# Optimization experiments

Hardware: AMD Instinct MI355X
Metric: run time of the kernel (lower is better)

## Reference

```python
import jax, jax.numpy as jnp
import numpy as np

N, E, MUL = 10000, 160000, 16
DIM = 9            # sum of 2l+1 for l=0..2
UV = 5             # 2*lmax+1
CONV = 9           # uv1 + uv2 - 1
ONE = CONV // 2 + 1
LOG2 = np.float32(np.log(2.0))


def _ssp(x):
    # ShiftedSoftPlus
    return jax.nn.softplus(x) - LOG2


def _build_a_w():
    # weight_align_matrix scaled by path_w ~ sqrt(2l+1): row l covers its (2l+1) block
    a = np.zeros((3, DIM), dtype=np.float32)
    off = 0
    for l in range(3):
        d = 2 * l + 1
        a[l, off:off + d] = np.sqrt(np.float32(d))
        off += d
    return jnp.asarray(a)


def setup_inputs() -> dict:
    key = jax.random.key(0)
    ks = jax.random.split(key, 14)
    inp = {
        "x": jax.random.normal(ks[0], (N, MUL, DIM), jnp.float32),
        "filter_sph": jax.random.normal(ks[1], (E, DIM), jnp.float32),
        "weight_in": jax.random.uniform(ks[2], (E, 8), jnp.float32),
        "edge_idx": jax.random.randint(ks[3], (2, E), 0, N),
        "Ux_re": jax.random.normal(ks[4], (DIM, UV, UV), jnp.float32),
        "Ux_im": jax.random.normal(ks[5], (DIM, UV, UV), jnp.float32),
        "Uf_re": jax.random.normal(ks[6], (DIM, UV, UV), jnp.float32),
        "Uf_im": jax.random.normal(ks[7], (DIM, UV, UV), jnp.float32),
        "Vout_re": jax.random.normal(ks[8], (CONV, ONE, DIM), jnp.float32),
        "Vout_im": jax.random.normal(ks[9], (CONV, ONE, DIM), jnp.float32),
        "W1": jax.random.normal(ks[10], (8, 64), jnp.float32),
        "W2": jax.random.normal(ks[11], (64, 64), jnp.float32),
        "W3": jax.random.normal(ks[12], (64, MUL * 3), jnp.float32),
        "a_w": _build_a_w(),
        "denominator": jnp.ones((1,), jnp.float32),
    }
    return inp


def _to_grid(coeff, U):
    # coeff [..., DIM] real; U [DIM, UV, UV] complex -> real grid [..., CONV, CONV]
    f = jnp.einsum('...d,duv->...uv', coeff.astype(U.dtype), U)
    pad = (CONV - UV) // 2
    cfg = [(0, 0)] * (f.ndim - 2) + [(pad, pad), (pad, pad)]
    fp = jnp.pad(f, cfg)
    fo = jnp.fft.ifftshift(fp, axes=(-2, -1))[..., :ONE]
    return jnp.fft.irfft2(fo, s=(CONV, CONV), axes=(-2, -1), norm='backward')


def reference(x, filter_sph, weight_in, edge_idx, Ux_re, Ux_im, Uf_re, Uf_im,
              Vout_re, Vout_im, W1, W2, W3, a_w, denominator):
    Ux = jax.lax.complex(Ux_re, Ux_im)
    Uf = jax.lax.complex(Uf_re, Uf_im)
    Vo = jax.lax.complex(Vout_re, Vout_im)
    edge_src = edge_idx[1]
    edge_dst = edge_idx[0]

    # node and filter signals on the CONVxCONV Fourier grid
    xf = _to_grid(x, Ux)                             # [N, MUL, 9, 9]
    yf = _to_grid(filter_sph[:, None, :], Uf)        # [E, 1, 9, 9]

    conv = xf[edge_src] * yf                         # [E, MUL, 9, 9]
    out_f = jnp.fft.rfft2(conv, axes=(-2, -1))       # [E, MUL, 9, 5] complex
    msg = jnp.einsum('emuv,uvd->emd', out_f, Vo).real  # ToSphericalBasis (hermitian input)

    # weight MLP (e3nn FullyConnectedNet: x @ W / sqrt(fan_in), ssp between)
    h = _ssp(weight_in @ W1 * (1.0 / np.sqrt(8.0, dtype=np.float32)))
    h = _ssp(h @ W2 * (1.0 / np.sqrt(64.0, dtype=np.float32)))
    w = (h @ W3 * (1.0 / np.sqrt(64.0, dtype=np.float32))).reshape(-1, MUL, 3)

    factor = jnp.einsum('emp,pd->emd', w, a_w)       # weight @ a_w
    message = msg * factor                           # [E, MUL, 9]

    out = jax.ops.segment_sum(message, edge_dst, num_segments=N)  # scatter-reduce sum
    return out / denominator[0]
```

## Files before the change

kernel.cpp:

```cpp
#include <hip/hip_runtime.h>
#include <math.h>

#define PI9 (2.0f * 3.14159265358979323846f / 9.0f)

typedef float f32x4 __attribute__((ext_vector_type(4)));
typedef unsigned short us8 __attribute__((ext_vector_type(8)));
typedef __bf16 bf16x8 __attribute__((ext_vector_type(8)));
typedef unsigned int u32x4 __attribute__((ext_vector_type(4)));

__device__ __forceinline__ float ssp_f(float x) {
  const float ax = fabsf(x);
  const float t = __expf(-ax);
  return fmaxf(x, 0.f) + __logf(1.f + t) - 0.69314718f;
}

__device__ __forceinline__ unsigned short f2bf(float f) {
  unsigned int u = __float_as_uint(f);
  unsigned int r = (u + 0x7FFFu + ((u >> 16) & 1u)) >> 16;
  return (unsigned short)r;
}

__device__ __forceinline__ float bfLO(unsigned int u) {
  return __uint_as_float(u << 16);
}
__device__ __forceinline__ float bfHI(unsigned int u) {
  return __uint_as_float(u & 0xffff0000u);
}

__global__ __launch_bounds__(256) void wconv_kernel(
    const float* __restrict__ W1, const float* __restrict__ W2,
    const float* __restrict__ W3, const float* __restrict__ a_w,
    const float* __restrict__ den, unsigned short* __restrict__ W1T,
    unsigned short* __restrict__ W2T, unsigned short* __restrict__ W3T,
    int* __restrict__ cnt, int N) {
  const int i = blockIdx.x * 256 + threadIdx.x;
  const float invden = 1.f / den[0];
  const float sc0 = a_w[0] * invden, sc1 = a_w[10] * invden, sc2 = a_w[22] * invden;
  const float rs8 = 0.35355339059327373f;
  if (i < N) cnt[i] = 0;
  if (i < 512) {
    const int col = i & 63, kk = i >> 6;
    W1T[col * 8 + kk] = f2bf(W1[kk * 64 + col] * rs8);
  } else if (i < 4608) {
    const int ii = i - 512;
    const int k = ii >> 6, j = ii & 63;
    W2T[j * 64 + ((((k >> 3) ^ (j & 7)) << 3)) + (k & 7)] = f2bf(W2[ii] * 0.125f);
  } else if (i < 7680) {
    const int ii = i - 4608;
    const int k = ii / 48, j = ii % 48;
    const int jm = j % 3;
    const float s = (jm == 0) ? sc0 : ((jm == 1) ? sc1 : sc2);
    W3T[j * 64 + ((((k >> 3) ^ (j & 7)) << 3)) + (k & 7)] = f2bf(W3[ii] * 0.125f * s);
  }
}

__device__ void precompute_body(
    int d, unsigned char* smem,
    const float* __restrict__ Ux_re, const float* __restrict__ Ux_im,
    const float* __restrict__ Uf_re, const float* __restrict__ Uf_im,
    const float* __restrict__ Vo_re, const float* __restrict__ Vo_im,
    float* __restrict__ CT) {
  float* G = (float*)smem;
  float* TL = (float*)(smem + 5840);
  float* cs9 = (float*)(smem + 8768);
  float* sn9 = (float*)(smem + 8816);
  const int t0 = threadIdx.x;

  if (t0 < 9) {
    float s, c;
    __sincosf(PI9 * (float)t0, &s, &c);
    cs9[t0] = c; sn9[t0] = s;
  }
  __syncthreads();

  for (int t = t0; t < 1458; t += 256) {
    const int which = t / 729, idx = t % 729;
    const int p = idx / 81, ab = idx % 81, a = ab / 9, b = ab % 9;
    const float* Ure = which ? Uf_re : Ux_re;
    const float* Uim = which ? Uf_im : Ux_im;
    float g = 0.f;
#pragma unroll
    for (int v = 0; v < 3; ++v) {
      const int uc = v + 2;
      float hre = 0.f, him = 0.f;
#pragma unroll
      for (int ui = 0; ui < 5; ++ui) {
        const int u = (ui + 7) % 9;
        const float re = Ure[p * 25 + ui * 5 + uc];
        const float im = Uim[p * 25 + ui * 5 + uc];
        const int k = (u * a) % 9;
        const float c = cs9[k], s = sn9[k];
        hre += re * c - im * s;
        him += re * s + im * c;
      }
      hre *= (1.f / 9.f); him *= (1.f / 9.f);
      if (v == 0) {
        g += hre;
      } else {
        const int k = (v * b) % 9;
        g += 2.f * (hre * cs9[k] - him * sn9[k]);
      }
    }
    G[which * 729 + p * 81 + ab] = g * (1.f / 9.f);
  }
  __syncthreads();

  for (int t = t0; t < 729; t += 256) {
    const int ab = t / 9, dd = t % 9, a = ab / 9, b = ab % 9;
    float acc = 0.f;
    for (int u = 0; u < 9; ++u)
      for (int v = 0; v < 5; ++v) {
        const int k = (u * a + v * b) % 9;
        acc += Vo_re[u * 45 + v * 9 + dd] * cs9[k]
             + Vo_im[u * 45 + v * 9 + dd] * sn9[k];
      }
    TL[ab * 9 + dd] = acc;
  }
  __syncthreads();

  if (t0 < 108) {
    const int p = t0 / 12, q = t0 % 12;
    float acc = 0.f;
    if (q < 9) {
      for (int ab = 0; ab < 81; ++ab)
        acc += G[p * 81 + ab] * G[729 + q * 81 + ab] * TL[ab * 9 + d];
    }
    CT[(d * 9 + p) * 12 + q] = acc;
  }
}

__device__ void mlp_body(
    int mblk, unsigned char* smem, const float* __restrict__ win,
    const unsigned short* __restrict__ W1T,
    const unsigned short* __restrict__ W2T,
    const unsigned short* __restrict__ W3T,
    unsigned short* __restrict__ w48b) {
  unsigned short* H1 = (unsigned short*)smem + ((threadIdx.x >> 6) * 1024);
  unsigned short* H2 = (unsigned short*)(smem + 8192) + ((threadIdx.x >> 6) * 1024);
  const int t = threadIdx.x;
  const int w = t >> 6, l = t & 63;
  const int n16 = l & 15, g = l >> 4;
  const bool isg0 = (g == 0);

#pragma unroll 1
  for (int rep = 0; rep < 2; ++rep) {
    const int e = mblk * 128 + rep * 64 + w * 16 + n16;

    bf16x8 Aw;
#pragma unroll
    for (int j = 0; j < 8; ++j) Aw[j] = (__bf16)0.f;
    if (isg0) {
      const float4 A = *(const float4*)(win + (size_t)e * 8);
      const float4 B = *(const float4*)(win + (size_t)e * 8 + 4);
      Aw[0] = (__bf16)A.x; Aw[1] = (__bf16)A.y;
      Aw[2] = (__bf16)A.z; Aw[3] = (__bf16)A.w;
      Aw[4] = (__bf16)B.x; Aw[5] = (__bf16)B.y;
      Aw[6] = (__bf16)B.z; Aw[7] = (__bf16)B.w;
    }
#pragma unroll
    for (int nt = 0; nt < 4; ++nt) {
      const int col = nt * 16 + n16;
      us8 bz;
#pragma unroll
      for (int j = 0; j < 8; ++j) bz[j] = 0;
      const us8 bw = isg0 ? *(const us8*)&W1T[col * 8] : bz;
      f32x4 acc = {0.f, 0.f, 0.f, 0.f};
      acc = __builtin_amdgcn_mfma_f32_16x16x32_bf16(
          Aw, __builtin_bit_cast(bf16x8, bw), acc, 0, 0, 0);
#pragma unroll
      for (int r = 0; r < 4; ++r) {
        const int e2 = g * 4 + r;
        const int k2 = nt * 16 + n16;
        H1[e2 * 64 + ((((k2 >> 3) ^ (e2 & 7)) << 3)) + (k2 & 7)] =
            f2bf(ssp_f(acc[r]));
      }
    }
    __builtin_amdgcn_wave_barrier();

    {
      const us8 a0 = *(const us8*)&H1[n16 * 64 + ((g ^ (n16 & 7)) << 3)];
      const us8 a1 = *(const us8*)&H1[n16 * 64 + (((g + 4) ^ (n16 & 7)) << 3)];
      float hh[16];
#pragma unroll
      for (int nt = 0; nt < 4; ++nt) {
        const int j = nt * 16 + n16;
        const us8 b0 = *(const us8*)&W2T[j * 64 + ((g ^ (j & 7)) << 3)];
        const us8 b1 = *(const us8*)&W2T[j * 64 + (((g + 4) ^ (j & 7)) << 3)];
        f32x4 acc = {0.f, 0.f, 0.f, 0.f};
        acc = __builtin_amdgcn_mfma_f32_16x16x32_bf16(
            __builtin_bit_cast(bf16x8, a0), __builtin_bit_cast(bf16x8, b0), acc, 0, 0, 0);
        acc = __builtin_amdgcn_mfma_f32_16x16x32_bf16(
            __builtin_bit_cast(bf16x8, a1), __builtin_bit_cast(bf16x8, b1), acc, 0, 0, 0);
#pragma unroll
        for (int r = 0; r < 4; ++r) hh[nt * 4 + r] = ssp_f(acc[r]);
      }
#pragma unroll
      for (int nt = 0; nt < 4; ++nt)
#pragma unroll
        for (int r = 0; r < 4; ++r) {
          const int e2 = g * 4 + r;
          const int k2 = nt * 16 + n16;
          H2[e2 * 64 + ((((k2 >> 3) ^ (e2 & 7)) << 3)) + (k2 & 7)] =
              f2bf(hh[nt * 4 + r]);
        }
    }
    __builtin_amdgcn_wave_barrier();

    {
      const us8 c0 = *(const us8*)&H2[n16 * 64 + ((g ^ (n16 & 7)) << 3)];
      const us8 c1 = *(const us8*)&H2[n16 * 64 + (((g + 4) ^ (n16 & 7)) << 3)];
      const int ebase = mblk * 128 + rep * 64 + w * 16 + g * 4;
#pragma unroll
      for (int nt = 0; nt < 3; ++nt) {
        const int o = nt * 16 + n16;
        const int om = o / 3, ol = o - om * 3;
        const us8 b0 = *(const us8*)&W3T[o * 64 + ((g ^ (o & 7)) << 3)];
        const us8 b1 = *(const us8*)&W3T[o * 64 + (((g + 4) ^ (o & 7)) << 3)];
        f32x4 acc = {0.f, 0.f, 0.f, 0.f};
        acc = __builtin_amdgcn_mfma_f32_16x16x32_bf16(
            __builtin_bit_cast(bf16x8, c0), __builtin_bit_cast(bf16x8, b0), acc, 0, 0, 0);
        acc = __builtin_amdgcn_mfma_f32_16x16x32_bf16(
            __builtin_bit_cast(bf16x8, c1), __builtin_bit_cast(bf16x8, b1), acc, 0, 0, 0);
#pragma unroll
        for (int r = 0; r < 4; ++r)
          w48b[(size_t)(ebase + r) * 64 + ol * 16 + om] = f2bf(acc[r]);
      }
    }
    __builtin_amdgcn_wave_barrier();
  }
}

__global__ __launch_bounds__(256) void prep_kernel(
    const float* __restrict__ win, const unsigned short* __restrict__ W1T,
    const unsigned short* __restrict__ W2T,
    const unsigned short* __restrict__ W3T,
    unsigned short* __restrict__ w48b,
    const int* __restrict__ dst, const int* __restrict__ src, int E,
    int* __restrict__ cnt, int2* __restrict__ slots2,
    const float* __restrict__ xsrc, int NR, unsigned short* __restrict__ xbf,
    const float* __restrict__ Ux_re, const float* __restrict__ Ux_im,
    const float* __restrict__ Uf_re, const float* __restrict__ Uf_im,
    const float* __restrict__ Vo_re, const float* __restrict__ Vo_im,
    float* __restrict__ CT, int nMlp, int nScat) {
  __shared__ __align__(16) unsigned char smem[16384];
  const int bid = blockIdx.x;
  if (bid < 9) {
    precompute_body(bid, smem, Ux_re, Ux_im, Uf_re, Uf_im, Vo_re, Vo_im, CT);
  } else if (bid < 9 + nMlp) {
    mlp_body(bid - 9, smem, win, W1T, W2T, W3T, w48b);
  } else if (bid < 9 + nMlp + nScat) {
    const int e = (bid - 9 - nMlp) * 256 + threadIdx.x;
    if (e < E) {
      const int d = dst[e];
      const int pos = atomicAdd(&cnt[d], 1);
      if (pos < 96) slots2[(size_t)d * 96 + pos] = make_int2(e, src[e]);
    }
  } else {
    const int r = (bid - 9 - nMlp - nScat) * 256 + threadIdx.x;
    if (r < NR) {
      const float* xp = xsrc + (size_t)r * 9;
      unsigned int u0 = (unsigned)f2bf(xp[0]) | ((unsigned)f2bf(xp[1]) << 16);
      unsigned int u1 = (unsigned)f2bf(xp[2]) | ((unsigned)f2bf(xp[3]) << 16);
      unsigned int u2 = (unsigned)f2bf(xp[4]) | ((unsigned)f2bf(xp[5]) << 16);
      unsigned int u3 = (unsigned)f2bf(xp[6]) | ((unsigned)f2bf(xp[7]) << 16);
      unsigned int u4 = (unsigned)f2bf(xp[8]);
      unsigned short* op = xbf + (size_t)r * 12;
      *(uint2*)op = make_uint2(u0, u1);
      *(uint2*)(op + 4) = make_uint2(u2, u3);
      *(uint2*)(op + 8) = make_uint2(u4, 0u);
    }
  }
}

__global__ __launch_bounds__(256) void node_kernel(
    const unsigned short* __restrict__ xbf, const float* __restrict__ filt,
    const int* __restrict__ cnt, const int2* __restrict__ slots2,
    const unsigned short* __restrict__ w48b, const float* __restrict__ CT,
    float* __restrict__ out, int N) {
  __shared__ __align__(16) unsigned short meL[4][2304];
  const int t = threadIdx.x, w = t >> 6, l = t & 63;
  const int n16 = l & 15, g = l >> 4;
  const int Ld = (n16 == 0) ? 0 : ((n16 < 4) ? 1 : 2);
  const bool dok = n16 < 9;
  const int drow = dok ? n16 : 0;
  const bool isg0 = (g == 0), isg1 = (g == 1);
  const int n = blockIdx.x * 4 + w;
  if (n >= N) return;

  int dT0, pT0, dT1, pT1, dT2, pT2, dT3, pT3, dT4, pT4, dT5, pT5;
  bool ok0, ok1, ok2, ok3, ok4, ok5;
  bf16x8 Bme0, Bme1, Bme2, Bme3, Bme4, Bme5;
#define MKB(tt, Bv, dv, pv, okv)                                             \
  {                                                                          \
    const int col = tt * 16 + n16;                                           \
    okv = (col < 81);                                                        \
    dv = okv ? col / 9 : 0;                                                  \
    pv = okv ? col % 9 : 0;                                                  \
    bf16x8 bv;                                                               \
    _Pragma("unroll")                                                        \
    for (int j = 0; j < 8; ++j) bv[j] = (__bf16)0.f;                         \
    if (okv) {                                                               \
      const float* cp = CT + col * 12;                                       \
      if (g == 0) {                                                          \
        const float4 ca = *(const float4*)cp;                                \
        const float4 cb = *(const float4*)(cp + 4);                          \
        bv[0] = (__bf16)ca.x; bv[1] = (__bf16)ca.y;                          \
        bv[2] = (__bf16)ca.z; bv[3] = (__bf16)ca.w;                          \
        bv[4] = (__bf16)cb.x; bv[5] = (__bf16)cb.y;                          \
        bv[6] = (__bf16)cb.z; bv[7] = (__bf16)cb.w;                          \
      } else if (g == 1) {                                                   \
        bv[0] = (__bf16)cp[8];                                               \
      }                                                                      \
    }                                                                        \
    Bv = bv;                                                                 \
  }
  MKB(0, Bme0, dT0, pT0, ok0); MKB(1, Bme1, dT1, pT1, ok1);
  MKB(2, Bme2, dT2, pT2, ok2); MKB(3, Bme3, dT3, pT3, ok3);
  MKB(4, Bme4, dT4, pT4, ok4); MKB(5, Bme5, dT5, pT5, ok5);
#undef MKB

  int deg = cnt[n];
  if (deg > 96) deg = 96;
  const int2* sl2 = slots2 + (size_t)n * 96;
  unsigned short* mlw = &meL[w][0];

  f32x4 accm = {0.f, 0.f, 0.f, 0.f};

  const int nb = (deg + 15) >> 4;
  for (int b = 0; b < nb; ++b) {
    const int base = b * 16;
    const int degb = (deg - base < 16) ? (deg - base) : 16;

    int esx = 0, esy = 0;
    if (n16 < degb) {
      const int2 v = sl2[base + n16];
      esx = v.x; esy = v.y;
    }
    bf16x8 Af;
#pragma unroll
    for (int j = 0; j < 8; ++j) Af[j] = (__bf16)0.f;
    if (n16 < degb) {
      const float* fp = filt + (size_t)esx * 9;
      if (g == 0) {
        const float4 fa = *(const float4*)fp;
        const float4 fb = *(const float4*)(fp + 4);
        Af[0] = (__bf16)fa.x; Af[1] = (__bf16)fa.y;
        Af[2] = (__bf16)fa.z; Af[3] = (__bf16)fa.w;
        Af[4] = (__bf16)fb.x; Af[5] = (__bf16)fb.y;
        Af[6] = (__bf16)fb.z; Af[7] = (__bf16)fb.w;
      } else if (g == 1) {
        Af[0] = (__bf16)fp[8];
      }
    }

#define MEMFMA(Bv, dv, pv, okv)                                              \
    {                                                                        \
      f32x4 a6 = {0.f, 0.f, 0.f, 0.f};                                       \
      a6 = __builtin_amdgcn_mfma_f32_16x16x32_bf16(Af, Bv, a6, 0, 0, 0);     \
      if (okv) {                                                             \
        _Pragma("unroll")                                                    \
        for (int r = 0; r < 4; ++r)                                          \
          mlw[(g * 4 + r) * 144 + dv * 16 + pv] = f2bf(a6[r]);               \
      }                                                                      \
    }
    MEMFMA(Bme0, dT0, pT0, ok0); MEMFMA(Bme1, dT1, pT1, ok1);
    MEMFMA(Bme2, dT2, pT2, ok2); MEMFMA(Bme3, dT3, pT3, ok3);
    MEMFMA(Bme4, dT4, pT4, ok4); MEMFMA(Bme5, dT5, pT5, ok5);
#undef MEMFMA
    __builtin_amdgcn_wave_barrier();

#define MSGLOAD(Q, QC, WV, il_)                                              \
    {                                                                        \
      const int e_ = __builtin_amdgcn_readlane(esx, (il_));                  \
      const int s_ = __builtin_amdgcn_readlane(esy, (il_));                  \
      const unsigned short* xrp_ = xbf + (size_t)s_ * 192 + n16 * 12;        \
      Q = *(const u32x4*)xrp_;                                               \
      QC = *(const unsigned int*)(xrp_ + 8);                                 \
      WV = *(const uint2*)(w48b + (size_t)e_ * 64 + Ld * 16 + g * 4);        \
    }

    u32x4 qA, qB;
    unsigned int qcA, qcB;
    uint2 wvA, wvB;
    MSGLOAD(qA, qcA, wvA, 0);
    if (degb > 1) MSGLOAD(qB, qcB, wvB, 1);

#pragma unroll 1
    for (int il = 0; il < degb; ++il) {
      const u32x4 q = qA;
      const unsigned int qc = qcA;
      const uint2 wv = wvA;
      qA = qB; qcA = qcB; wvA = wvB;
      if (il + 2 < degb) MSGLOAD(qB, qcB, wvB, il + 2);

      const unsigned short* mr = mlw + il * 144 + drow * 16;
      const u32x4 mdv = *(const u32x4*)mr;
      const unsigned int md4 = (*(const unsigned int*)(mr + 8)) & 0xffffu;

      u32x4 av;
      av[0] = isg0 ? q[0] : (isg1 ? qc : 0u);
      av[1] = isg0 ? q[1] : 0u;
      av[2] = isg0 ? q[2] : 0u;
      av[3] = isg0 ? q[3] : 0u;
      u32x4 bv;
      bv[0] = isg0 ? mdv[0] : (isg1 ? md4 : 0u);
      bv[1] = isg0 ? mdv[1] : 0u;
      bv[2] = isg0 ? mdv[2] : 0u;
      bv[3] = isg0 ? mdv[3] : 0u;

      f32x4 c1 = {0.f, 0.f, 0.f, 0.f};
      c1 = __builtin_amdgcn_mfma_f32_16x16x32_bf16(
          __builtin_bit_cast(bf16x8, av), __builtin_bit_cast(bf16x8, bv),
          c1, 0, 0, 0);
      accm[0] = fmaf(c1[0], bfLO(wv.x), accm[0]);
      accm[1] = fmaf(c1[1], bfHI(wv.x), accm[1]);
      accm[2] = fmaf(c1[2], bfLO(wv.y), accm[2]);
      accm[3] = fmaf(c1[3], bfHI(wv.y), accm[3]);
    }
#undef MSGLOAD
    __builtin_amdgcn_wave_barrier();
  }

  if (dok) {
    float* op = out + (size_t)n * 144 + (g * 4) * 9 + n16;
    op[0]  = accm[0];
    op[9]  = accm[1];
    op[18] = accm[2];
    op[27] = accm[3];
  }
}

extern "C" void kernel_launch(void* const* d_in, const int* in_sizes, int n_in,
                              void* d_out, int out_size, void* d_ws, size_t ws_size,
                              hipStream_t stream) {
  const float* x      = (const float*)d_in[0];
  const float* filt   = (const float*)d_in[1];
  const float* win    = (const float*)d_in[2];
  const int*   eidx   = (const int*)d_in[3];
  const float* Ux_re  = (const float*)d_in[4];
  const float* Ux_im  = (const float*)d_in[5];
  const float* Uf_re  = (const float*)d_in[6];
  const float* Uf_im  = (const float*)d_in[7];
  const float* Vo_re  = (const float*)d_in[8];
  const float* Vo_im  = (const float*)d_in[9];
  const float* W1     = (const float*)d_in[10];
  const float* W2     = (const float*)d_in[11];
  const float* W3     = (const float*)d_in[12];
  const float* a_w    = (const float*)d_in[13];
  const float* den    = (const float*)d_in[14];
  float* out = (float*)d_out;

  const int N = in_sizes[0] / 144;
  const int E = in_sizes[3] / 2;
  const int NR = N * 16;
  const int* dst = eidx;
  const int* src = eidx + E;

  char* wsb = (char*)d_ws;
  const size_t off_cnt  = 8192;
  const size_t off_slot = off_cnt + 40960;
  const size_t off_w48  = off_slot + (size_t)N * 96 * 8;
  const size_t off_xbf  = off_w48 + (size_t)E * 64 * 2;
  const size_t off_w1t  = off_xbf + (size_t)NR * 12 * 2;
  const size_t off_w2t  = off_w1t + 512 * 2;
  const size_t off_w3t  = off_w2t + 4096 * 2;

  float*          CT    = (float*)wsb;
  int*            cnt   = (int*)(wsb + off_cnt);
  int2*           slot2 = (int2*)(wsb + off_slot);
  unsigned short* w48b  = (unsigned short*)(wsb + off_w48);
  unsigned short* xbf   = (unsigned short*)(wsb + off_xbf);
  unsigned short* W1T   = (unsigned short*)(wsb + off_w1t);
  unsigned short* W2T   = (unsigned short*)(wsb + off_w2t);
  unsigned short* W3T   = (unsigned short*)(wsb + off_w3t);

  const int nMlp  = E / 128;
  const int nScat = (E + 255) / 256;
  const int nXc   = (NR + 255) / 256;

  wconv_kernel<<<(N + 255) / 256, 256, 0, stream>>>(
      W1, W2, W3, a_w, den, W1T, W2T, W3T, cnt, N);
  prep_kernel<<<9 + nMlp + nScat + nXc, 256, 0, stream>>>(
      win, W1T, W2T, W3T, w48b,
      dst, src, E, cnt, slot2,
      x, NR, xbf,
      Ux_re, Ux_im, Uf_re, Uf_im, Vo_re, Vo_im, CT, nMlp, nScat);
  node_kernel<<<(N + 3) / 4, 256, 0, stream>>>(
      xbf, filt, cnt, slot2, w48b, CT, out, N);
}
```

Before: 73.87 us.

## Split MLP blocks finer and software-pipeline node message loop with dual accumulators

The MLP part of prep_kernel now handles 64 edges per block instead of looping twice over 128, which doubles the number of MLP blocks for more parallelism. In node_kernel, the edge slot indices for the next 16-edge batch are prefetched before the barrier. The per-edge message loop is unrolled by two, with the LDS filter loads folded into the prefetch and two independent accumulators to break the FMA dependency chain. This adds register pressure and more blocks in exchange for better latency hiding.

```diff
diff --git a/kernel.cpp b/kernel.cpp
--- a/kernel.cpp
+++ b/kernel.cpp
@@ -142,91 +142,87 @@
   const int n16 = l & 15, g = l >> 4;
   const bool isg0 = (g == 0);
 
-#pragma unroll 1
-  for (int rep = 0; rep < 2; ++rep) {
-    const int e = mblk * 128 + rep * 64 + w * 16 + n16;
-
-    bf16x8 Aw;
-#pragma unroll
-    for (int j = 0; j < 8; ++j) Aw[j] = (__bf16)0.f;
-    if (isg0) {
-      const float4 A = *(const float4*)(win + (size_t)e * 8);
-      const float4 B = *(const float4*)(win + (size_t)e * 8 + 4);
-      Aw[0] = (__bf16)A.x; Aw[1] = (__bf16)A.y;
-      Aw[2] = (__bf16)A.z; Aw[3] = (__bf16)A.w;
-      Aw[4] = (__bf16)B.x; Aw[5] = (__bf16)B.y;
-      Aw[6] = (__bf16)B.z; Aw[7] = (__bf16)B.w;
-    }
+  const int e = mblk * 64 + w * 16 + n16;
+
+  bf16x8 Aw;
+#pragma unroll
+  for (int j = 0; j < 8; ++j) Aw[j] = (__bf16)0.f;
+  if (isg0) {
+    const float4 A = *(const float4*)(win + (size_t)e * 8);
+    const float4 B = *(const float4*)(win + (size_t)e * 8 + 4);
+    Aw[0] = (__bf16)A.x; Aw[1] = (__bf16)A.y;
+    Aw[2] = (__bf16)A.z; Aw[3] = (__bf16)A.w;
+    Aw[4] = (__bf16)B.x; Aw[5] = (__bf16)B.y;
+    Aw[6] = (__bf16)B.z; Aw[7] = (__bf16)B.w;
+  }
+#pragma unroll
+  for (int nt = 0; nt < 4; ++nt) {
+    const int col = nt * 16 + n16;
+    us8 bz;
+#pragma unroll
+    for (int j = 0; j < 8; ++j) bz[j] = 0;
+    const us8 bw = isg0 ? *(const us8*)&W1T[col * 8] : bz;
+    f32x4 acc = {0.f, 0.f, 0.f, 0.f};
+    acc = __builtin_amdgcn_mfma_f32_16x16x32_bf16(
+        Aw, __builtin_bit_cast(bf16x8, bw), acc, 0, 0, 0);
+#pragma unroll
+    for (int r = 0; r < 4; ++r) {
+      const int e2 = g * 4 + r;
+      const int k2 = nt * 16 + n16;
+      H1[e2 * 64 + ((((k2 >> 3) ^ (e2 & 7)) << 3)) + (k2 & 7)] =
+          f2bf(ssp_f(acc[r]));
+    }
+  }
+  __builtin_amdgcn_wave_barrier();
+
+  {
+    const us8 a0 = *(const us8*)&H1[n16 * 64 + ((g ^ (n16 & 7)) << 3)];
+    const us8 a1 = *(const us8*)&H1[n16 * 64 + (((g + 4) ^ (n16 & 7)) << 3)];
+    float hh[16];
 #pragma unroll
     for (int nt = 0; nt < 4; ++nt) {
-      const int col = nt * 16 + n16;
-      us8 bz;
-#pragma unroll
-      for (int j = 0; j < 8; ++j) bz[j] = 0;
-      const us8 bw = isg0 ? *(const us8*)&W1T[col * 8] : bz;
+      const int j = nt * 16 + n16;
+      const us8 b0 = *(const us8*)&W2T[j * 64 + ((g ^ (j & 7)) << 3)];
+      const us8 b1 = *(const us8*)&W2T[j * 64 + (((g + 4) ^ (j & 7)) << 3)];
       f32x4 acc = {0.f, 0.f, 0.f, 0.f};
       acc = __builtin_amdgcn_mfma_f32_16x16x32_bf16(
-          Aw, __builtin_bit_cast(bf16x8, bw), acc, 0, 0, 0);
+          __builtin_bit_cast(bf16x8, a0), __builtin_bit_cast(bf16x8, b0), acc, 0, 0, 0);
+      acc = __builtin_amdgcn_mfma_f32_16x16x32_bf16(
+          __builtin_bit_cast(bf16x8, a1), __builtin_bit_cast(bf16x8, b1), acc, 0, 0, 0);
+#pragma unroll
+      for (int r = 0; r < 4; ++r) hh[nt * 4 + r] = ssp_f(acc[r]);
+    }
+#pragma unroll
+    for (int nt = 0; nt < 4; ++nt)
 #pragma unroll
       for (int r = 0; r < 4; ++r) {
         const int e2 = g * 4 + r;
         const int k2 = nt * 16 + n16;
-        H1[e2 * 64 + ((((k2 >> 3) ^ (e2 & 7)) << 3)) + (k2 & 7)] =
-            f2bf(ssp_f(acc[r]));
+        H2[e2 * 64 + ((((k2 >> 3) ^ (e2 & 7)) << 3)) + (k2 & 7)] =
+            f2bf(hh[nt * 4 + r]);
       }
-    }
-    __builtin_amdgcn_wave_barrier();
-
-    {
-      const us8 a0 = *(const us8*)&H1[n16 * 64 + ((g ^ (n16 & 7)) << 3)];
-      const us8 a1 = *(const us8*)&H1[n16 * 64 + (((g + 4) ^ (n16 & 7)) << 3)];
-      float hh[16];
-#pragma unroll
-      for (int nt = 0; nt < 4; ++nt) {
-        const int j = nt * 16 + n16;
-        const us8 b0 = *(const us8*)&W2T[j * 64 + ((g ^ (j & 7)) << 3)];
-        const us8 b1 = *(const us8*)&W2T[j * 64 + (((g + 4) ^ (j & 7)) << 3)];
-        f32x4 acc = {0.f, 0.f, 0.f, 0.f};
-        acc = __builtin_amdgcn_mfma_f32_16x16x32_bf16(
-            __builtin_bit_cast(bf16x8, a0), __builtin_bit_cast(bf16x8, b0), acc, 0, 0, 0);
-        acc = __builtin_amdgcn_mfma_f32_16x16x32_bf16(
-            __builtin_bit_cast(bf16x8, a1), __builtin_bit_cast(bf16x8, b1), acc, 0, 0, 0);
-#pragma unroll
-        for (int r = 0; r < 4; ++r) hh[nt * 4 + r] = ssp_f(acc[r]);
-      }
-#pragma unroll
-      for (int nt = 0; nt < 4; ++nt)
-#pragma unroll
-        for (int r = 0; r < 4; ++r) {
-          const int e2 = g * 4 + r;
-          const int k2 = nt * 16 + n16;
-          H2[e2 * 64 + ((((k2 >> 3) ^ (e2 & 7)) << 3)) + (k2 & 7)] =
-              f2bf(hh[nt * 4 + r]);
-        }
-    }
-    __builtin_amdgcn_wave_barrier();
-
-    {
-      const us8 c0 = *(const us8*)&H2[n16 * 64 + ((g ^ (n16 & 7)) << 3)];
-      const us8 c1 = *(const us8*)&H2[n16 * 64 + (((g + 4) ^ (n16 & 7)) << 3)];
-      const int ebase = mblk * 128 + rep * 64 + w * 16 + g * 4;
-#pragma unroll
-      for (int nt = 0; nt < 3; ++nt) {
-        const int o = nt * 16 + n16;
-        const int om = o / 3, ol = o - om * 3;
-        const us8 b0 = *(const us8*)&W3T[o * 64 + ((g ^ (o & 7)) << 3)];
-        const us8 b1 = *(const us8*)&W3T[o * 64 + (((g + 4) ^ (o & 7)) << 3)];
-        f32x4 acc = {0.f, 0.f, 0.f, 0.f};
-        acc = __builtin_amdgcn_mfma_f32_16x16x32_bf16(
-            __builtin_bit_cast(bf16x8, c0), __builtin_bit_cast(bf16x8, b0), acc, 0, 0, 0);
-        acc = __builtin_amdgcn_mfma_f32_16x16x32_bf16(
-            __builtin_bit_cast(bf16x8, c1), __builtin_bit_cast(bf16x8, b1), acc, 0, 0, 0);
-#pragma unroll
-        for (int r = 0; r < 4; ++r)
-          w48b[(size_t)(ebase + r) * 64 + ol * 16 + om] = f2bf(acc[r]);
-      }
-    }
-    __builtin_amdgcn_wave_barrier();
+  }
+  __builtin_amdgcn_wave_barrier();
+
+  {
+    const us8 c0 = *(const us8*)&H2[n16 * 64 + ((g ^ (n16 & 7)) << 3)];
+    const us8 c1 = *(const us8*)&H2[n16 * 64 + (((g + 4) ^ (n16 & 7)) << 3)];
+    const int ebase = mblk * 64 + w * 16 + g * 4;
+#pragma unroll
+    for (int nt = 0; nt < 3; ++nt) {
+      const int o = nt * 16 + n16;
+      const int om = o / 3, ol = o - om * 3;
+      const us8 b0 = *(const us8*)&W3T[o * 64 + ((g ^ (o & 7)) << 3)];
+      const us8 b1 = *(const us8*)&W3T[o * 64 + (((g + 4) ^ (o & 7)) << 3)];
+      f32x4 acc = {0.f, 0.f, 0.f, 0.f};
+      acc = __builtin_amdgcn_mfma_f32_16x16x32_bf16(
+          __builtin_bit_cast(bf16x8, c0), __builtin_bit_cast(bf16x8, b0), acc, 0, 0, 0);
+      acc = __builtin_amdgcn_mfma_f32_16x16x32_bf16(
+          __builtin_bit_cast(bf16x8, c1), __builtin_bit_cast(bf16x8, b1), acc, 0, 0, 0);
+#pragma unroll
+      for (int r = 0; r < 4; ++r)
+        w48b[(size_t)(ebase + r) * 64 + ol * 16 + om] = f2bf(acc[r]);
+    }
   }
 }
 
@@ -324,18 +320,21 @@
   const int2* sl2 = slots2 + (size_t)n * 96;
   unsigned short* mlw = &meL[w][0];
 
-  f32x4 accm = {0.f, 0.f, 0.f, 0.f};
+  f32x4 acc0 = {0.f, 0.f, 0.f, 0.f};
+  f32x4 acc1 = {0.f, 0.f, 0.f, 0.f};
 
   const int nb = (deg + 15) >> 4;
+
+  int esx = 0, esy = 0;
+  if (n16 < deg) {
+    const int2 v = sl2[n16];
+    esx = v.x; esy = v.y;
+  }
+
   for (int b = 0; b < nb; ++b) {
     const int base = b * 16;
     const int degb = (deg - base < 16) ? (deg - base) : 16;
 
-    int esx = 0, esy = 0;
-    if (n16 < degb) {
-      const int2 v = sl2[base + n16];
-      esx = v.x; esy = v.y;
-    }
     bf16x8 Af;
 #pragma unroll
     for (int j = 0; j < 8; ++j) Af[j] = (__bf16)0.f;
@@ -367,9 +366,15 @@
     MEMFMA(Bme2, dT2, pT2, ok2); MEMFMA(Bme3, dT3, pT3, ok3);
     MEMFMA(Bme4, dT4, pT4, ok4); MEMFMA(Bme5, dT5, pT5, ok5);
 #undef MEMFMA
+
+    int esx_n = 0, esy_n = 0;
+    if (b + 1 < nb && base + 16 + n16 < deg) {
+      const int2 v = sl2[base + 16 + n16];
+      esx_n = v.x; esy_n = v.y;
+    }
     __builtin_amdgcn_wave_barrier();
 
-#define MSGLOAD(Q, QC, WV, il_)                                              \
+#define MSGLOAD(Q, QC, WV, MD, MD4, il_)                                     \
     {                                                                        \
       const int e_ = __builtin_amdgcn_readlane(esx, (il_));                  \
       const int s_ = __builtin_amdgcn_readlane(esy, (il_));                  \
@@ -377,56 +382,67 @@
       Q = *(const u32x4*)xrp_;                                               \
       QC = *(const unsigned int*)(xrp_ + 8);                                 \
       WV = *(const uint2*)(w48b + (size_t)e_ * 64 + Ld * 16 + g * 4);        \
-    }
-
-    u32x4 qA, qB;
-    unsigned int qcA, qcB;
+      const unsigned short* mr_ = mlw + (il_) * 144 + drow * 16;             \
+      MD = *(const u32x4*)mr_;                                               \
+      MD4 = (*(const unsigned int*)(mr_ + 8)) & 0xffffu;                     \
+    }
+
+#define MSGBODY(Q, QC, WV, MD, MD4, ACC)                                     \
+    {                                                                        \
+      u32x4 av;                                                              \
+      av[0] = isg0 ? Q[0] : (isg1 ? QC : 0u);                                \
+      av[1] = isg0 ? Q[1] : 0u;                                              \
+      av[2] = isg0 ? Q[2] : 0u;                                              \
+      av[3] = isg0 ? Q[3] : 0u;                                              \
+      u32x4 bv;                                                              \
+      bv[0] = isg0 ? MD[0] : (isg1 ? MD4 : 0u);                              \
+      bv[1] = isg0 ? MD[1] : 0u;                                             \
+      bv[2] = isg0 ? MD[2] : 0u;                                             \
+      bv[3] = isg0 ? MD[3] : 0u;                                             \
+      f32x4 c1 = {0.f, 0.f, 0.f, 0.f};                                       \
+      c1 = __builtin_amdgcn_mfma_f32_16x16x32_bf16(                          \
+          __builtin_bit_cast(bf16x8, av), __builtin_bit_cast(bf16x8, bv),    \
+          c1, 0, 0, 0);                                                      \
+      ACC[0] = fmaf(c1[0], bfLO(WV.x), ACC[0]);                              \
+      ACC[1] = fmaf(c1[1], bfHI(WV.x), ACC[1]);                              \
+      ACC[2] = fmaf(c1[2], bfLO(WV.y), ACC[2]);                              \
+      ACC[3] = fmaf(c1[3], bfHI(WV.y), ACC[3]);                              \
+    }
+
+    u32x4 qA, qB, mdA, mdB;
+    unsigned int qcA, qcB, md4A, md4B;
     uint2 wvA, wvB;
-    MSGLOAD(qA, qcA, wvA, 0);
-    if (degb > 1) MSGLOAD(qB, qcB, wvB, 1);
-
+    MSGLOAD(qA, qcA, wvA, mdA, md4A, 0);
+    if (degb > 1) MSGLOAD(qB, qcB, wvB, mdB, md4B, 1);
+
+    int il = 0;
 #pragma unroll 1
-    for (int il = 0; il < degb; ++il) {
-      const u32x4 q = qA;
-      const unsigned int qc = qcA;
-      const uint2 wv = wvA;
-      qA = qB; qcA = qcB; wvA = wvB;
-      if (il + 2 < degb) MSGLOAD(qB, qcB, wvB, il + 2);
-
-      const unsigned short* mr = mlw + il * 144 + drow * 16;
-      const u32x4 mdv = *(const u32x4*)mr;
-      const unsigned int md4 = (*(const unsigned int*)(mr + 8)) & 0xffffu;
-
-      u32x4 av;
-      av[0] = isg0 ? q[0] : (isg1 ? qc : 0u);
-      av[1] = isg0 ? q[1] : 0u;
-      av[2] = isg0 ? q[2] : 0u;
-      av[3] = isg0 ? q[3] : 0u;
-      u32x4 bv;
-      bv[0] = isg0 ? mdv[0] : (isg1 ? md4 : 0u);
-      bv[1] = isg0 ? mdv[1] : 0u;
-      bv[2] = isg0 ? mdv[2] : 0u;
-      bv[3] = isg0 ? mdv[3] : 0u;
-
-      f32x4 c1 = {0.f, 0.f, 0.f, 0.f};
-      c1 = __builtin_amdgcn_mfma_f32_16x16x32_bf16(
-          __builtin_bit_cast(bf16x8, av), __builtin_bit_cast(bf16x8, bv),
-          c1, 0, 0, 0);
-      accm[0] = fmaf(c1[0], bfLO(wv.x), accm[0]);
-      accm[1] = fmaf(c1[1], bfHI(wv.x), accm[1]);
-      accm[2] = fmaf(c1[2], bfLO(wv.y), accm[2]);
-      accm[3] = fmaf(c1[3], bfHI(wv.y), accm[3]);
-    }
+    for (; il + 2 <= degb; il += 2) {
+      const u32x4 q0 = qA, m0 = mdA;
+      const unsigned int qc0 = qcA, m40 = md4A;
+      const uint2 wv0 = wvA;
+      const u32x4 q1 = qB, m1 = mdB;
+      const unsigned int qc1 = qcB, m41 = md4B;
+      const uint2 wv1 = wvB;
+      if (il + 2 < degb) MSGLOAD(qA, qcA, wvA, mdA, md4A, il + 2);
+      if (il + 3 < degb) MSGLOAD(qB, qcB, wvB, mdB, md4B, il + 3);
+      MSGBODY(q0, qc0, wv0, m0, m40, acc0);
+      MSGBODY(q1, qc1, wv1, m1, m41, acc1);
+    }
+    if (il < degb) MSGBODY(qA, qcA, wvA, mdA, md4A, acc0);
 #undef MSGLOAD
+#undef MSGBODY
     __builtin_amdgcn_wave_barrier();
+
+    esx = esx_n; esy = esy_n;
   }
 
   if (dok) {
     float* op = out + (size_t)n * 144 + (g * 4) * 9 + n16;
-    op[0]  = accm[0];
-    op[9]  = accm[1];
-    op[18] = accm[2];
-    op[27] = accm[3];
+    op[0]  = acc0[0] + acc1[0];
+    op[9]  = acc0[1] + acc1[1];
+    op[18] = acc0[2] + acc1[2];
+    op[27] = acc0[3] + acc1[3];
   }
 }
 
@@ -474,7 +490,7 @@
   unsigned short* W2T   = (unsigned short*)(wsb + off_w2t);
   unsigned short* W3T   = (unsigned short*)(wsb + off_w3t);
 
-  const int nMlp  = E / 128;
+  const int nMlp  = E / 64;
   const int nScat = (E + 255) / 256;
   const int nXc   = (NR + 255) / 256;
 
```

Measured after the change: 77.77 us. 5.3% more time.
